# Kernel tuning notes

Measured on AMD Instinct MI355X. Metric: run time of the kernel, lower is better.

## Reference

```python
import jax, jax.numpy as jnp
import numpy as np
import math

N, B, S = 2048, 4, 1024
SFZ, IFZ, H, A = 384, 256, 8, 64
LN_EPS = 1e-5


def setup_inputs() -> dict:
    key = jax.random.key(0)
    ks = jax.random.split(key, 12)
    x = jax.random.normal(ks[0], (N, IFZ), dtype=jnp.float32)
    emb = jax.random.normal(ks[1], (B, S, SFZ), dtype=jnp.float32)
    mask = jax.random.randint(ks[2], (B, S), 0, 2).astype(bool)
    batch = jnp.sort(jax.random.randint(ks[3], (N,), 0, B)).astype(jnp.int64)
    sc = 1.0 / math.sqrt(IFZ)
    scs = 1.0 / math.sqrt(SFZ)
    Wq = jax.random.normal(ks[4], (IFZ, H * A), dtype=jnp.float32) * sc
    Wk = jax.random.normal(ks[5], (SFZ, H * A), dtype=jnp.float32) * scs
    Wv = jax.random.normal(ks[6], (SFZ, H * A), dtype=jnp.float32) * scs
    Wg = jax.random.normal(ks[7], (IFZ, H * A), dtype=jnp.float32) * sc
    bg = jnp.zeros((H * A,), dtype=jnp.float32)
    Wback = jax.random.normal(ks[8], (H * A, IFZ), dtype=jnp.float32) / math.sqrt(H * A)
    bback = jnp.zeros((IFZ,), dtype=jnp.float32)
    gamma = jnp.ones((IFZ,), dtype=jnp.float32)
    beta = jnp.zeros((IFZ,), dtype=jnp.float32)
    return {"x": x, "packed_sequence_emb": emb, "packed_sequence_mask": mask,
            "batch": batch, "Wq": Wq, "Wk": Wk, "Wv": Wv, "Wg": Wg, "bg": bg,
            "Wback": Wback, "bback": bback, "gamma": gamma, "beta": beta}


def _masked_softmax(scores, mask):
    # scores: [N,S,H], mask: [N,S,1] bool; softmax over S with padded entries zeroed
    neg = jnp.finfo(scores.dtype).min
    s = jnp.where(mask, scores, neg)
    s = s - jnp.max(s, axis=1, keepdims=True)
    e = jnp.exp(s) * mask
    return e / (jnp.sum(e, axis=1, keepdims=True) + 1e-9)


def reference(x, packed_sequence_emb, packed_sequence_mask, batch,
              Wq, Wk, Wv, Wg, bg, Wback, bback, gamma, beta):
    scale = math.sqrt(A)
    q = (x @ Wq).reshape(N, H, A)                               # [N,H,A]
    k = (packed_sequence_emb @ Wk).reshape(B, S, H, A)          # [B,S,H,A]
    v = (packed_sequence_emb @ Wv).reshape(B, S, H, A)
    # scores per (node, candidate-batch), then gather node's own batch entry;
    # avoids materializing k[batch] of shape [N,S,H,A]
    scores_all = jnp.einsum('nha,bsha->nbsh', q, k) / scale     # [N,B,S,H]
    idx = batch[:, None, None, None].astype(jnp.int32)
    scores = jnp.take_along_axis(scores_all, idx, axis=1)[:, 0]  # [N,S,H]
    bmask = packed_sequence_mask[batch][..., None]               # [N,S,1]
    w = _masked_softmax(scores, bmask)                           # [N,S,H]
    feat_all = jnp.einsum('nsh,bsha->nbha', w, v)                # [N,B,H,A]
    feat = jnp.take_along_axis(feat_all, idx, axis=1)[:, 0]      # [N,H,A]
    gate = jax.nn.sigmoid(x @ Wg + bg).reshape(N, H, A)
    new = (gate * feat).reshape(N, H * A) @ Wback + bback        # [N,IFZ]
    y = math.sqrt(2.0) * x + new
    mu = jnp.mean(y, axis=-1, keepdims=True)
    var = jnp.mean((y - mu) ** 2, axis=-1, keepdims=True)
    out = (y - mu) * jax.lax.rsqrt(var + LN_EPS) * gamma + beta
    seq_aa_logits = jnp.sum(scores[..., :2], axis=-1)            # [N,S]
    return out, seq_aa_logits
```

## Files before the change

### kernel.cpp

```cpp
#include <hip/hip_runtime.h>
#include <hip/hip_bf16.h>

#define NND 2048
#define BBATCH 4
#define SS 1024
#define SFZ 384
#define IFZ 256
#define HH 8
#define AA 64
#define HA 512
#define NBX 48
#define NSPL 8

typedef __attribute__((ext_vector_type(8))) short bf16x8;
typedef __attribute__((ext_vector_type(4))) float f32x4;

__device__ __forceinline__ unsigned short f2bf(float f) {
    union { float f; unsigned u; } a; a.f = f;
    unsigned r = a.u + 0x7fffu + ((a.u >> 16) & 1u);
    return (unsigned short)(r >> 16);
}
__device__ __forceinline__ float bf2f(unsigned short u) {
    return __uint_as_float((unsigned)u << 16);
}

__device__ __forceinline__ bf16x8 cvt8(const float* __restrict__ p) {
    const float4 f0 = *(const float4*)p;
    const float4 f1 = *(const float4*)(p + 4);
    bf16x8 o;
    o[0] = (short)f2bf(f0.x); o[1] = (short)f2bf(f0.y);
    o[2] = (short)f2bf(f0.z); o[3] = (short)f2bf(f0.w);
    o[4] = (short)f2bf(f1.x); o[5] = (short)f2bf(f1.y);
    o[6] = (short)f2bf(f1.z); o[7] = (short)f2bf(f1.w);
    return o;
}

__device__ __forceinline__ void tile_transpose(
    const float* __restrict__ src, unsigned short* __restrict__ dst,
    int K, int N, int kt, int nt, int t)
{
    __shared__ unsigned short tile[64][65];
    const int k0 = kt * 64, n0 = nt * 64;
    const int tr = t >> 6, tc = t & 63;
    #pragma unroll
    for (int r = 0; r < 16; ++r)
        tile[tr + r*4][tc] = f2bf(src[(size_t)(k0 + tr + r*4) * N + n0 + tc]);
    __syncthreads();
    #pragma unroll
    for (int r = 0; r < 16; ++r)
        dst[(size_t)(n0 + tr + r*4) * K + k0 + tc] = tile[tc][tr + r*4];
}

__global__ __launch_bounds__(256) void prep_kernel(
    const float* __restrict__ Wk, const float* __restrict__ Wv,
    const float* __restrict__ Wq, const float* __restrict__ Wg,
    const float* __restrict__ Wback,
    const void* __restrict__ mask_raw, const void* __restrict__ batch_raw,
    unsigned short* __restrict__ WkT, unsigned short* __restrict__ WvT,
    unsigned short* __restrict__ WqT, unsigned short* __restrict__ WgT,
    unsigned short* __restrict__ WbackT,
    float* __restrict__ mask_f, int* __restrict__ seg)
{
    const int bx = blockIdx.x, t = threadIdx.x;
    if (bx < 48)  { tile_transpose(Wk, WkT, SFZ, HA, bx/8, bx%8, t); return; }
    if (bx < 96)  { const int i = bx-48;  tile_transpose(Wv, WvT, SFZ, HA, i/8, i%8, t); return; }
    if (bx < 128) { const int i = bx-96;  tile_transpose(Wq, WqT, IFZ, HA, i/8, i%8, t); return; }
    if (bx < 160) { const int i = bx-128; tile_transpose(Wg, WgT, IFZ, HA, i/8, i%8, t); return; }
    if (bx < 192) { const int i = bx-160; tile_transpose(Wback, WbackT, HA, IFZ, i/4, i%4, t); return; }
    __shared__ int fl[4];
    __shared__ int fb;
    __shared__ int cnt[4];
    if (t < 4) { fl[t] = 0; cnt[t] = 0; }
    if (t == 0) fb = 0;
    __syncthreads();
    const unsigned char*  mb = (const unsigned char*)mask_raw;
    const unsigned short* mh = (const unsigned short*)mask_raw;
    const unsigned int*   mw = (const unsigned int*)mask_raw;
    int f0 = 0, f1 = 0, f2 = 0, f3 = 0;
    for (int i = t; i < 2048; i += 256) {
        unsigned short h = mh[i];
        if (h == 0x3f80u) f0 = 1;
        if ((i & 1) == 0 && h != 0) f1 = 1;
    }
    for (int i = t; i < 4096; i += 256)
        if ((i & 3) != 0 && mb[i] != 0) f2 = 1;
    for (int i = t; i < 1024; i += 256)
        if ((i & 1) != 0 && mw[i] != 0) f3 = 1;
    const int* bw = (const int*)batch_raw;
    int f4 = 0;
    for (int i = t + 1; i < 2048; i += 256)
        if (bw[i] < bw[i-1]) f4 = 1;
    if (f0) atomicOr(&fl[0], 1);
    if (f1) atomicOr(&fl[1], 1);
    if (f2) atomicOr(&fl[2], 1);
    if (f3) atomicOr(&fl[3], 1);
    if (f4) atomicOr(&fb, 1);
    __syncthreads();
    int mode;
    if (fl[0])      mode = fl[1] ? 1 : 0;
    else if (fl[2]) mode = 2;
    else if (fl[3]) mode = 3;
    else            mode = 4;
    for (int s = t; s < BBATCH*SS; s += 256) {
        int m;
        switch (mode) {
            case 0:  m = (mw[s]   != 0); break;
            case 1:  m = (mh[s]   != 0); break;
            case 2:  m = (mb[s]   != 0); break;
            case 3:  m = (mw[s]   != 0); break;
            default: m = (mw[2*s] != 0); break;
        }
        mask_f[s] = m ? 1.0f : 0.0f;
    }
    const int b64 = fb;
    for (int i = t; i < NND; i += 256) {
        const int bv = (b64 ? bw[2*i] : bw[i]) & 3;
        atomicAdd(&cnt[bv], 1);
    }
    __syncthreads();
    if (t == 0) {
        int s = 0;
        for (int b = 0; b < 4; ++b) { seg[2*b] = s; s += cnt[b]; seg[2*b+1] = s; }
    }
}

__global__ __launch_bounds__(256) void proj_mfma(
    const float* __restrict__ emb, const float* __restrict__ x,
    const unsigned short* __restrict__ WkT, const unsigned short* __restrict__ WvT,
    const unsigned short* __restrict__ WqT, const unsigned short* __restrict__ WgT,
    const float* __restrict__ bg,
    unsigned short* __restrict__ k_blk, unsigned short* __restrict__ vT_bf,
    unsigned short* __restrict__ q_bf, float* __restrict__ gate_ws)
{
    __shared__ unsigned short v_l[16][520];
    const int t = threadIdx.x, w = t >> 6, lane = t & 63;
    const int m16 = lane & 15, quad = lane >> 4;
    const int bx = blockIdx.x;
    if (bx < 512) {
        const int r0 = (bx >> 1) * 16;
        const int b = r0 >> 10, srow = r0 & (SS - 1);
        const float* ap = emb + (size_t)(r0 + m16) * SFZ + quad * 8;
        bf16x8 af[12];
        #pragma unroll
        for (int j = 0; j < 12; ++j) af[j] = cvt8(ap + j * 32);
        if ((bx & 1) == 0) {
            #pragma unroll
            for (int nt = 0; nt < 8; ++nt) {
                const int n0 = w * 128 + nt * 16;
                const unsigned short* bp = WkT + (size_t)(n0 + m16) * SFZ + quad * 8;
                f32x4 d = (f32x4){0.f, 0.f, 0.f, 0.f};
                #pragma unroll
                for (int j = 0; j < 12; ++j)
                    d = __builtin_amdgcn_mfma_f32_16x16x32_bf16(af[j], *(const bf16x8*)(bp + j * 32), d, 0, 0, 0);
                const int head = n0 >> 6, coff = (n0 & 63) + m16;
                unsigned short* kb = k_blk + (((size_t)(b * HH + head)) * SS) * 64 + coff;
                #pragma unroll
                for (int r = 0; r < 4; ++r)
                    kb[(size_t)(srow + quad * 4 + r) * 64] = f2bf(d[r]);
            }
        } else {
            #pragma unroll
            for (int nt = 0; nt < 8; ++nt) {
                const int n0 = w * 128 + nt * 16;
                const unsigned short* bp = WvT + (size_t)(n0 + m16) * SFZ + quad * 8;
                f32x4 d = (f32x4){0.f, 0.f, 0.f, 0.f};
                #pragma unroll
                for (int j = 0; j < 12; ++j)
                    d = __builtin_amdgcn_mfma_f32_16x16x32_bf16(af[j], *(const bf16x8*)(bp + j * 32), d, 0, 0, 0);
                #pragma unroll
                for (int r = 0; r < 4; ++r)
                    v_l[quad * 4 + r][n0 + m16] = f2bf(d[r]);
            }
            __syncthreads();
            for (int c = t; c < HA; c += 256) {
                unsigned short tmp[16];
                #pragma unroll
                for (int s = 0; s < 16; ++s) tmp[s] = v_l[s][c];
                unsigned short* dst = vT_bf + ((size_t)b * HA + c) * SS + srow;
                *(uint4*)dst       = ((const uint4*)tmp)[0];
                *(uint4*)(dst + 8) = ((const uint4*)tmp)[1];
            }
        }
    } else {
        const int i = bx - 512;
        const int r0 = (i >> 2) * 16;
        const int tensor = (i & 3) >> 1, half = i & 1;
        const unsigned short* Wt = tensor ? WgT : WqT;
        const float* ap = x + (size_t)(r0 + m16) * IFZ + quad * 8;
        bf16x8 af[8];
        #pragma unroll
        for (int j = 0; j < 8; ++j) af[j] = cvt8(ap + j * 32);
        #pragma unroll
        for (int nt = 0; nt < 4; ++nt) {
            const int n0 = half * 256 + w * 64 + nt * 16;
            const unsigned short* bp = Wt + (size_t)(n0 + m16) * IFZ + quad * 8;
            f32x4 d = (f32x4){0.f, 0.f, 0.f, 0.f};
            #pragma unroll
            for (int j = 0; j < 8; ++j)
                d = __builtin_amdgcn_mfma_f32_16x16x32_bf16(af[j], *(const bf16x8*)(bp + j * 32), d, 0, 0, 0);
            if (tensor == 0) {
                #pragma unroll
                for (int r = 0; r < 4; ++r)
                    q_bf[(size_t)(r0 + quad * 4 + r) * HA + n0 + m16] = f2bf(d[r]);
            } else {
                const float bgv = bg[n0 + m16];
                #pragma unroll
                for (int r = 0; r < 4; ++r)
                    gate_ws[(size_t)(r0 + quad * 4 + r) * HA + n0 + m16] =
                        1.f / (1.f + __expf(-(d[r] + bgv)));
            }
        }
    }
}

__global__ __launch_bounds__(256) void attn_kernel(
    const unsigned short* __restrict__ k_blk, const unsigned short* __restrict__ vT_bf,
    const unsigned short* __restrict__ q_bf, const float* __restrict__ mask_f,
    const int* __restrict__ seg, unsigned short* __restrict__ part_O,
    float2* __restrict__ part_ml, float* __restrict__ out_logits)
{
    __shared__ unsigned short P_lds[4][16][136];
    const int bid = blockIdx.x;
    const int xcd = bid & 7;
    const int b   = xcd >> 1;
    const int idx = (bid >> 3) * 2 + (xcd & 1);
    const int z    = idx & 15;
    const int xblk = idx >> 4;
    const int hz    = z >> 3;
    const int split = z & 7;
    const int n0 = seg[2*b] + xblk * 16;
    const int nend = seg[2*b + 1];
    if (n0 >= nend) return;
    const int nvalid = min(16, nend - n0);

    const int t = threadIdx.x;
    const int w = t >> 6, lane = t & 63;
    const int m16 = lane & 15, quad = lane >> 4;
    const int h = hz * 4 + w;
    const int s0 = split * 128;

    int nq = n0 + m16; if (nq >= nend) nq = nend - 1;
    const unsigned short* qp = q_bf + (size_t)nq * HA + h * AA + quad * 8;
    const bf16x8 qa0 = *(const bf16x8*)qp;
    const bf16x8 qa1 = *(const bf16x8*)(qp + 32);

    const unsigned short* kb = k_blk + ((size_t)(b * HH + h)) * SS * 64;
    const unsigned short* vb = vT_bf + ((size_t)b * HA + h * AA) * SS;
    unsigned short (*Pw)[136] = P_lds[w];

    float msk[8];
    #pragma unroll
    for (int st = 0; st < 8; ++st)
        msk[st] = mask_f[b * SS + s0 + st * 16 + m16];

    f32x4 d[8];
    #pragma unroll
    for (int st = 0; st < 8; ++st) {
        const unsigned short* kp = kb + (size_t)(s0 + st * 16 + m16) * 64 + quad * 8;
        const bf16x8 b0 = *(const bf16x8*)kp;
        const bf16x8 b1 = *(const bf16x8*)(kp + 32);
        f32x4 acc = (f32x4){0.f, 0.f, 0.f, 0.f};
        acc = __builtin_amdgcn_mfma_f32_16x16x32_bf16(qa0, b0, acc, 0, 0, 0);
        acc = __builtin_amdgcn_mfma_f32_16x16x32_bf16(qa1, b1, acc, 0, 0, 0);
        #pragma unroll
        for (int r = 0; r < 4; ++r) acc[r] *= 0.125f;
        d[st] = acc;
    }
    if (hz == 0 && w == 0) {
        const unsigned short* qp1 = q_bf + (size_t)nq * HA + AA + quad * 8;
        const bf16x8 qb0 = *(const bf16x8*)qp1;
        const bf16x8 qb1 = *(const bf16x8*)(qp1 + 32);
        const unsigned short* kb1 = k_blk + ((size_t)(b * HH + 1)) * SS * 64;
        #pragma unroll
        for (int st = 0; st < 8; ++st) {
            const unsigned short* kp = kb1 + (size_t)(s0 + st * 16 + m16) * 64 + quad * 8;
            f32x4 acc = (f32x4){0.f, 0.f, 0.f, 0.f};
            acc = __builtin_amdgcn_mfma_f32_16x16x32_bf16(qb0, *(const bf16x8*)kp, acc, 0, 0, 0);
            acc = __builtin_amdgcn_mfma_f32_16x16x32_bf16(qb1, *(const bf16x8*)(kp + 32), acc, 0, 0, 0);
            #pragma unroll
            for (int r = 0; r < 4; ++r) {
                const int node = quad * 4 + r;
                if (node < nvalid)
                    out_logits[(size_t)(n0 + node) * SS + s0 + st * 16 + m16] =
                        d[st][r] + acc[r] * 0.125f;
            }
        }
    }
    float m_s[4], l_s[4];
    #pragma unroll
    for (int r = 0; r < 4; ++r) {
        float mx = -3.0e38f;
        #pragma unroll
        for (int st = 0; st < 8; ++st)
            mx = (msk[st] > 0.5f) ? fmaxf(mx, d[st][r]) : mx;
        mx = fmaxf(mx, __shfl_xor(mx, 1));
        mx = fmaxf(mx, __shfl_xor(mx, 2));
        mx = fmaxf(mx, __shfl_xor(mx, 4));
        mx = fmaxf(mx, __shfl_xor(mx, 8));
        m_s[r] = mx;
        float cs = 0.f;
        #pragma unroll
        for (int st = 0; st < 8; ++st) {
            const float e = (msk[st] > 0.5f) ? __expf(d[st][r] - mx) : 0.f;
            d[st][r] = e;
            cs += e;
        }
        cs += __shfl_xor(cs, 1);
        cs += __shfl_xor(cs, 2);
        cs += __shfl_xor(cs, 4);
        cs += __shfl_xor(cs, 8);
        l_s[r] = cs;
    }
    #pragma unroll
    for (int st = 0; st < 8; ++st)
        #pragma unroll
        for (int r = 0; r < 4; ++r)
            Pw[quad * 4 + r][st * 16 + m16] = f2bf(d[st][r]);
    f32x4 facc[4];
    #pragma unroll
    for (int a = 0; a < 4; ++a) facc[a] = (f32x4){0.f, 0.f, 0.f, 0.f};
    #pragma unroll
    for (int sub = 0; sub < 4; ++sub) {
        const bf16x8 pa = *(const bf16x8*)&Pw[m16][sub * 32 + quad * 8];
        const unsigned short* vp0 = vb + (size_t)m16 * SS + s0 + sub * 32 + quad * 8;
        #pragma unroll
        for (int a = 0; a < 4; ++a) {
            const bf16x8 vfr = *(const bf16x8*)(vp0 + (size_t)(a * 16) * SS);
            facc[a] = __builtin_amdgcn_mfma_f32_16x16x32_bf16(pa, vfr, facc[a], 0, 0, 0);
        }
    }
    unsigned short* po = part_O + (size_t)split * NND * HA;
    #pragma unroll
    for (int a = 0; a < 4; ++a)
        #pragma unroll
        for (int r = 0; r < 4; ++r) {
            const int row = quad * 4 + r;
            if (row < nvalid)
                po[(size_t)(n0 + row) * HA + h * AA + a * 16 + m16] = f2bf(facc[a][r]);
        }
    if (m16 == 0) {
        #pragma unroll
        for (int r = 0; r < 4; ++r) {
            const int row = quad * 4 + r;
            if (row < nvalid)
                part_ml[(size_t)split * NND * HH + (size_t)(n0 + row) * HH + h] =
                    make_float2(m_s[r], l_s[r]);
        }
    }
}

__global__ __launch_bounds__(256) void back_ln_fused(
    const unsigned short* __restrict__ part_O, const float2* __restrict__ part_ml,
    const float* __restrict__ gate_ws, const unsigned short* __restrict__ WbackT,
    const float* __restrict__ x, const float* __restrict__ bback,
    const float* __restrict__ gamma, const float* __restrict__ beta,
    float* __restrict__ out)
{
    __shared__ float coef[NSPL][8][8];
    __shared__ unsigned short gf_l[8][520];
    __shared__ float nl[8][260];
    const int t = threadIdx.x, w = t >> 6, lane = t & 63;
    const int m16 = lane & 15, quad = lane >> 4;
    const int r0 = blockIdx.x * 8;
    if (t < 64) {
        const int row = t >> 3, h = t & 7, n = r0 + row;
        float2 ml[NSPL];
        #pragma unroll
        for (int s = 0; s < NSPL; ++s)
            ml[s] = part_ml[(size_t)s * NND * HH + (size_t)n * HH + h];
        float M = -3.0e38f;
        #pragma unroll
        for (int s = 0; s < NSPL; ++s) M = fmaxf(M, ml[s].x);
        float L = 0.f;
        float e[NSPL];
        #pragma unroll
        for (int s = 0; s < NSPL; ++s) { e[s] = __expf(ml[s].x - M); L += ml[s].y * e[s]; }
        const float invL = 1.f / (L + 1e-9f);
        #pragma unroll
        for (int s = 0; s < NSPL; ++s) coef[s][row][h] = e[s] * invL;
    }
    __syncthreads();
    #pragma unroll
    for (int it = 0; it < 4; ++it) {
        const int i = (t + it * 256) * 4;
        const int row = i >> 9, c = i & (HA - 1), h = c >> 6;
        const int n = r0 + row;
        float4 o = make_float4(0.f, 0.f, 0.f, 0.f);
        #pragma unroll
        for (int s = 0; s < NSPL; ++s) {
            const ushort4 p = *(const ushort4*)&part_O[(size_t)s * NND * HA + (size_t)n * HA + c];
            const float cf = coef[s][row][h];
            o.x = fmaf(bf2f(p.x), cf, o.x); o.y = fmaf(bf2f(p.y), cf, o.y);
            o.z = fmaf(bf2f(p.z), cf, o.z); o.w = fmaf(bf2f(p.w), cf, o.w);
        }
        const float4 g = *(const float4*)&gate_ws[(size_t)n * HA + c];
        ushort4 ob;
        ob.x = f2bf(g.x * o.x); ob.y = f2bf(g.y * o.y);
        ob.z = f2bf(g.z * o.z); ob.w = f2bf(g.w * o.w);
        *(ushort4*)&gf_l[row][c] = ob;
    }
    __syncthreads();
    bf16x8 af[16];
    #pragma unroll
    for (int j = 0; j < 16; ++j)
        af[j] = *(const bf16x8*)&gf_l[m16 & 7][quad * 8 + j * 32];
    #pragma unroll
    for (int nt = 0; nt < 4; ++nt) {
        const int n0 = w * 64 + nt * 16;
        const unsigned short* bp = WbackT + (size_t)(n0 + m16) * HA + quad * 8;
        f32x4 d = (f32x4){0.f, 0.f, 0.f, 0.f};
        #pragma unroll
        for (int j = 0; j < 16; ++j)
            d = __builtin_amdgcn_mfma_f32_16x16x32_bf16(af[j], *(const bf16x8*)(bp + j * 32), d, 0, 0, 0);
        const float bb = bback[n0 + m16];
        #pragma unroll
        for (int r = 0; r < 4; ++r) {
            const int rr = quad * 4 + r;
            if (rr < 8) nl[rr][n0 + m16] = d[r] + bb;
        }
    }
    __syncthreads();
    const int row = t >> 5, li = t & 31;
    const float* xr = x + (size_t)(r0 + row) * IFZ;
    float yv[8];
    float s1 = 0.f, s2 = 0.f;
    #pragma unroll
    for (int j = 0; j < 8; ++j) {
        const int c = li + j * 32;
        const float v = fmaf(1.41421356237309515f, xr[c], nl[row][c]);
        yv[j] = v; s1 += v; s2 += v * v;
    }
    #pragma unroll
    for (int off = 16; off >= 1; off >>= 1) {
        s1 += __shfl_xor(s1, off);
        s2 += __shfl_xor(s2, off);
    }
    const float mu  = s1 * (1.f / IFZ);
    const float var = s2 * (1.f / IFZ) - mu * mu;
    const float rv  = rsqrtf(var + 1e-5f);
    float* orow = out + (size_t)(r0 + row) * IFZ;
    #pragma unroll
    for (int j = 0; j < 8; ++j) {
        const int c = li + j * 32;
        orow[c] = (yv[j] - mu) * rv * gamma[c] + beta[c];
    }
}

extern "C" void kernel_launch(void* const* d_in, const int* in_sizes, int n_in,
                              void* d_out, int out_size, void* d_ws, size_t ws_size,
                              hipStream_t stream) {
    const float* x     = (const float*)d_in[0];
    const float* emb   = (const float*)d_in[1];
    const void*  mraw  = d_in[2];
    const void*  braw  = d_in[3];
    const float* Wq    = (const float*)d_in[4];
    const float* Wk    = (const float*)d_in[5];
    const float* Wv    = (const float*)d_in[6];
    const float* Wg    = (const float*)d_in[7];
    const float* bg    = (const float*)d_in[8];
    const float* Wback = (const float*)d_in[9];
    const float* bback = (const float*)d_in[10];
    const float* gamma = (const float*)d_in[11];
    const float* beta  = (const float*)d_in[12];

    char* ws = (char*)d_ws;
    const size_t MB = 1048576;
    size_t off = 0;
    float*          mask_f  = (float*)(ws + off);  off += 16384;
    int*            seg     = (int*)(ws + off);    off += 16384;
    unsigned short* WkT     = (unsigned short*)(ws + off); off += 393216;
    unsigned short* WvT     = (unsigned short*)(ws + off); off += 393216;
    unsigned short* WqT     = (unsigned short*)(ws + off); off += 262144;
    unsigned short* WgT     = (unsigned short*)(ws + off); off += 262144;
    unsigned short* WbackT  = (unsigned short*)(ws + off); off += 262144;
    unsigned short* k_blk   = (unsigned short*)(ws + off); off += 4*MB;
    unsigned short* vT_bf   = (unsigned short*)(ws + off); off += 4*MB;
    unsigned short* q_bf    = (unsigned short*)(ws + off); off += 2*MB;
    float*          gate_ws = (float*)(ws + off); off += 4*MB;
    unsigned short* part_O  = (unsigned short*)(ws + off); off += 16*MB;
    float2*         part_ml = (float2*)(ws + off); off += 1*MB;

    float* out        = (float*)d_out;
    float* out_logits = out + (size_t)NND * IFZ;

    hipLaunchKernelGGL(prep_kernel, dim3(193), dim3(256), 0, stream,
                       Wk, Wv, Wq, Wg, Wback, mraw, braw,
                       WkT, WvT, WqT, WgT, WbackT, mask_f, seg);
    hipLaunchKernelGGL(proj_mfma, dim3(1024), dim3(256), 0, stream,
                       emb, x, WkT, WvT, WqT, WgT, bg, k_blk, vT_bf, q_bf, gate_ws);
    hipLaunchKernelGGL(attn_kernel, dim3(BBATCH * NBX * 16), dim3(256), 0, stream,
                       k_blk, vT_bf, q_bf, mask_f, seg, part_O, part_ml, out_logits);
    hipLaunchKernelGGL(back_ln_fused, dim3(NND / 8), dim3(256), 0, stream,
                       part_O, part_ml, gate_ws, WbackT, x, bback, gamma, beta, out);
}
```

Baseline: 204.3 us.

## Halve attention splits with online softmax; rebalance projection and back-LN grids

```diff
diff --git a/kernel.cpp b/kernel.cpp
--- a/kernel.cpp
+++ b/kernel.cpp
@@ -10,7 +10,7 @@
 #define AA 64
 #define HA 512
 #define NBX 48
-#define NSPL 8
+#define NSPL 4
 
 typedef __attribute__((ext_vector_type(8))) short bf16x8;
 typedef __attribute__((ext_vector_type(4))) float f32x4;
@@ -136,17 +136,19 @@
     const int t = threadIdx.x, w = t >> 6, lane = t & 63;
     const int m16 = lane & 15, quad = lane >> 4;
     const int bx = blockIdx.x;
-    if (bx < 512) {
-        const int r0 = (bx >> 1) * 16;
+    if (bx < 1024) {
+        const int r0 = (bx >> 2) * 16;
+        const int sub = bx & 3;
+        const int tensor = sub >> 1, chalf = sub & 1;
         const int b = r0 >> 10, srow = r0 & (SS - 1);
         const float* ap = emb + (size_t)(r0 + m16) * SFZ + quad * 8;
         bf16x8 af[12];
         #pragma unroll
         for (int j = 0; j < 12; ++j) af[j] = cvt8(ap + j * 32);
-        if ((bx & 1) == 0) {
-            #pragma unroll
-            for (int nt = 0; nt < 8; ++nt) {
-                const int n0 = w * 128 + nt * 16;
+        if (tensor == 0) {
+            #pragma unroll
+            for (int nt = 0; nt < 4; ++nt) {
+                const int n0 = chalf * 256 + w * 64 + nt * 16;
                 const unsigned short* bp = WkT + (size_t)(n0 + m16) * SFZ + quad * 8;
                 f32x4 d = (f32x4){0.f, 0.f, 0.f, 0.f};
                 #pragma unroll
@@ -160,8 +162,8 @@
             }
         } else {
             #pragma unroll
-            for (int nt = 0; nt < 8; ++nt) {
-                const int n0 = w * 128 + nt * 16;
+            for (int nt = 0; nt < 4; ++nt) {
+                const int n0 = chalf * 256 + w * 64 + nt * 16;
                 const unsigned short* bp = WvT + (size_t)(n0 + m16) * SFZ + quad * 8;
                 f32x4 d = (f32x4){0.f, 0.f, 0.f, 0.f};
                 #pragma unroll
@@ -172,7 +174,8 @@
                     v_l[quad * 4 + r][n0 + m16] = f2bf(d[r]);
             }
             __syncthreads();
-            for (int c = t; c < HA; c += 256) {
+            {
+                const int c = chalf * 256 + t;
                 unsigned short tmp[16];
                 #pragma unroll
                 for (int s = 0; s < 16; ++s) tmp[s] = v_l[s][c];
@@ -182,7 +185,7 @@
             }
         }
     } else {
-        const int i = bx - 512;
+        const int i = bx - 1024;
         const int r0 = (i >> 2) * 16;
         const int tensor = (i & 3) >> 1, half = i & 1;
         const unsigned short* Wt = tensor ? WgT : WqT;
@@ -224,10 +227,10 @@
     const int xcd = bid & 7;
     const int b   = xcd >> 1;
     const int idx = (bid >> 3) * 2 + (xcd & 1);
-    const int z    = idx & 15;
-    const int xblk = idx >> 4;
-    const int hz    = z >> 3;
-    const int split = z & 7;
+    const int z    = idx & 7;
+    const int xblk = idx >> 3;
+    const int hz    = z >> 2;
+    const int split = z & 3;
     const int n0 = seg[2*b] + xblk * 16;
     const int nend = seg[2*b + 1];
     if (n0 >= nend) return;
@@ -237,7 +240,6 @@
     const int w = t >> 6, lane = t & 63;
     const int m16 = lane & 15, quad = lane >> 4;
     const int h = hz * 4 + w;
-    const int s0 = split * 128;
 
     int nq = n0 + m16; if (nq >= nend) nq = nend - 1;
     const unsigned short* qp = q_bf + (size_t)nq * HA + h * AA + quad * 8;
@@ -248,96 +250,120 @@
     const unsigned short* vb = vT_bf + ((size_t)b * HA + h * AA) * SS;
     unsigned short (*Pw)[136] = P_lds[w];
 
-    float msk[8];
-    #pragma unroll
-    for (int st = 0; st < 8; ++st)
-        msk[st] = mask_f[b * SS + s0 + st * 16 + m16];
-
-    f32x4 d[8];
-    #pragma unroll
-    for (int st = 0; st < 8; ++st) {
-        const unsigned short* kp = kb + (size_t)(s0 + st * 16 + m16) * 64 + quad * 8;
-        const bf16x8 b0 = *(const bf16x8*)kp;
-        const bf16x8 b1 = *(const bf16x8*)(kp + 32);
-        f32x4 acc = (f32x4){0.f, 0.f, 0.f, 0.f};
-        acc = __builtin_amdgcn_mfma_f32_16x16x32_bf16(qa0, b0, acc, 0, 0, 0);
-        acc = __builtin_amdgcn_mfma_f32_16x16x32_bf16(qa1, b1, acc, 0, 0, 0);
-        #pragma unroll
-        for (int r = 0; r < 4; ++r) acc[r] *= 0.125f;
-        d[st] = acc;
-    }
-    if (hz == 0 && w == 0) {
+    const bool do_logits = (hz == 0 && w == 0);
+    bf16x8 qb0, qb1;
+    const unsigned short* kb1 = k_blk + ((size_t)(b * HH + 1)) * SS * 64;
+    if (do_logits) {
         const unsigned short* qp1 = q_bf + (size_t)nq * HA + AA + quad * 8;
-        const bf16x8 qb0 = *(const bf16x8*)qp1;
-        const bf16x8 qb1 = *(const bf16x8*)(qp1 + 32);
-        const unsigned short* kb1 = k_blk + ((size_t)(b * HH + 1)) * SS * 64;
+        qb0 = *(const bf16x8*)qp1;
+        qb1 = *(const bf16x8*)(qp1 + 32);
+    }
+
+    float m_s[4], l_s[4];
+    #pragma unroll
+    for (int r = 0; r < 4; ++r) { m_s[r] = -3.0e38f; l_s[r] = 0.f; }
+    f32x4 facc[4];
+    #pragma unroll
+    for (int a = 0; a < 4; ++a) facc[a] = (f32x4){0.f, 0.f, 0.f, 0.f};
+
+    for (int ch = 0; ch < 2; ++ch) {
+        const int s0 = split * 256 + ch * 128;
+        float msk[8];
+        #pragma unroll
+        for (int st = 0; st < 8; ++st)
+            msk[st] = mask_f[b * SS + s0 + st * 16 + m16];
+        f32x4 d[8];
         #pragma unroll
         for (int st = 0; st < 8; ++st) {
-            const unsigned short* kp = kb1 + (size_t)(s0 + st * 16 + m16) * 64 + quad * 8;
+            const unsigned short* kp = kb + (size_t)(s0 + st * 16 + m16) * 64 + quad * 8;
+            const bf16x8 b0 = *(const bf16x8*)kp;
+            const bf16x8 b1 = *(const bf16x8*)(kp + 32);
             f32x4 acc = (f32x4){0.f, 0.f, 0.f, 0.f};
-            acc = __builtin_amdgcn_mfma_f32_16x16x32_bf16(qb0, *(const bf16x8*)kp, acc, 0, 0, 0);
-            acc = __builtin_amdgcn_mfma_f32_16x16x32_bf16(qb1, *(const bf16x8*)(kp + 32), acc, 0, 0, 0);
-            #pragma unroll
-            for (int r = 0; r < 4; ++r) {
-                const int node = quad * 4 + r;
-                if (node < nvalid)
-                    out_logits[(size_t)(n0 + node) * SS + s0 + st * 16 + m16] =
-                        d[st][r] + acc[r] * 0.125f;
-            }
-        }
-    }
-    float m_s[4], l_s[4];
-    #pragma unroll
-    for (int r = 0; r < 4; ++r) {
-        float mx = -3.0e38f;
+            acc = __builtin_amdgcn_mfma_f32_16x16x32_bf16(qa0, b0, acc, 0, 0, 0);
+            acc = __builtin_amdgcn_mfma_f32_16x16x32_bf16(qa1, b1, acc, 0, 0, 0);
+            #pragma unroll
+            for (int r = 0; r < 4; ++r) acc[r] *= 0.125f;
+            d[st] = acc;
+        }
+        if (do_logits) {
+            #pragma unroll
+            for (int st = 0; st < 8; ++st) {
+                const unsigned short* kp = kb1 + (size_t)(s0 + st * 16 + m16) * 64 + quad * 8;
+                f32x4 acc = (f32x4){0.f, 0.f, 0.f, 0.f};
+                acc = __builtin_amdgcn_mfma_f32_16x16x32_bf16(qb0, *(const bf16x8*)kp, acc, 0, 0, 0);
+                acc = __builtin_amdgcn_mfma_f32_16x16x32_bf16(qb1, *(const bf16x8*)(kp + 32), acc, 0, 0, 0);
+                #pragma unroll
+                for (int r = 0; r < 4; ++r) {
+                    const int node = quad * 4 + r;
+                    if (node < nvalid)
+                        out_logits[(size_t)(n0 + node) * SS + s0 + st * 16 + m16] =
+                            d[st][r] + acc[r] * 0.125f;
+                }
+            }
+        }
+        float al[4];
+        #pragma unroll
+        for (int r = 0; r < 4; ++r) {
+            float mx = -3.0e38f;
+            #pragma unroll
+            for (int st = 0; st < 8; ++st)
+                mx = (msk[st] > 0.5f) ? fmaxf(mx, d[st][r]) : mx;
+            mx = fmaxf(mx, __shfl_xor(mx, 1));
+            mx = fmaxf(mx, __shfl_xor(mx, 2));
+            mx = fmaxf(mx, __shfl_xor(mx, 4));
+            mx = fmaxf(mx, __shfl_xor(mx, 8));
+            const float mnew = fmaxf(m_s[r], mx);
+            al[r] = __expf(m_s[r] - mnew);
+            m_s[r] = mnew;
+            float cs = 0.f;
+            #pragma unroll
+            for (int st = 0; st < 8; ++st) {
+                const float e = (msk[st] > 0.5f) ? __expf(d[st][r] - mnew) : 0.f;
+                d[st][r] = e;
+                cs += e;
+            }
+            cs += __shfl_xor(cs, 1);
+            cs += __shfl_xor(cs, 2);
+            cs += __shfl_xor(cs, 4);
+            cs += __shfl_xor(cs, 8);
+            l_s[r] = l_s[r] * al[r] + cs;
+        }
         #pragma unroll
         for (int st = 0; st < 8; ++st)
-            mx = (msk[st] > 0.5f) ? fmaxf(mx, d[st][r]) : mx;
-        mx = fmaxf(mx, __shfl_xor(mx, 1));
-        mx = fmaxf(mx, __shfl_xor(mx, 2));
-        mx = fmaxf(mx, __shfl_xor(mx, 4));
-        mx = fmaxf(mx, __shfl_xor(mx, 8));
-        m_s[r] = mx;
-        float cs = 0.f;
-        #pragma unroll
-        for (int st = 0; st < 8; ++st) {
-            const float e = (msk[st] > 0.5f) ? __expf(d[st][r] - mx) : 0.f;
-            d[st][r] = e;
-            cs += e;
-        }
-        cs += __shfl_xor(cs, 1);
-        cs += __shfl_xor(cs, 2);
-        cs += __shfl_xor(cs, 4);
-        cs += __shfl_xor(cs, 8);
-        l_s[r] = cs;
-    }
-    #pragma unroll
-    for (int st = 0; st < 8; ++st)
+            #pragma unroll
+            for (int r = 0; r < 4; ++r)
+                Pw[quad * 4 + r][st * 16 + m16] = f2bf(d[st][r]);
+        #pragma unroll
+        for (int a = 0; a < 4; ++a)
+            #pragma unroll
+            for (int r = 0; r < 4; ++r) facc[a][r] *= al[r];
+        #pragma unroll
+        for (int sub = 0; sub < 4; ++sub) {
+            const bf16x8 pa = *(const bf16x8*)&Pw[m16][sub * 32 + quad * 8];
+            const unsigned short* vp0 = vb + (size_t)m16 * SS + s0 + sub * 32 + quad * 8;
+            #pragma unroll
+            for (int a = 0; a < 4; ++a) {
+                const bf16x8 vfr = *(const bf16x8*)(vp0 + (size_t)(a * 16) * SS);
+                facc[a] = __builtin_amdgcn_mfma_f32_16x16x32_bf16(pa, vfr, facc[a], 0, 0, 0);
+            }
+        }
+    }
+    #pragma unroll
+    for (int a = 0; a < 4; ++a)
         #pragma unroll
         for (int r = 0; r < 4; ++r)
-            Pw[quad * 4 + r][st * 16 + m16] = f2bf(d[st][r]);
-    f32x4 facc[4];
-    #pragma unroll
-    for (int a = 0; a < 4; ++a) facc[a] = (f32x4){0.f, 0.f, 0.f, 0.f};
-    #pragma unroll
-    for (int sub = 0; sub < 4; ++sub) {
-        const bf16x8 pa = *(const bf16x8*)&Pw[m16][sub * 32 + quad * 8];
-        const unsigned short* vp0 = vb + (size_t)m16 * SS + s0 + sub * 32 + quad * 8;
-        #pragma unroll
-        for (int a = 0; a < 4; ++a) {
-            const bf16x8 vfr = *(const bf16x8*)(vp0 + (size_t)(a * 16) * SS);
-            facc[a] = __builtin_amdgcn_mfma_f32_16x16x32_bf16(pa, vfr, facc[a], 0, 0, 0);
-        }
-    }
-    unsigned short* po = part_O + (size_t)split * NND * HA;
-    #pragma unroll
-    for (int a = 0; a < 4; ++a)
-        #pragma unroll
-        for (int r = 0; r < 4; ++r) {
-            const int row = quad * 4 + r;
-            if (row < nvalid)
-                po[(size_t)(n0 + row) * HA + h * AA + a * 16 + m16] = f2bf(facc[a][r]);
-        }
+            Pw[quad * 4 + r][a * 16 + m16] = f2bf(facc[a][r]);
+    {
+        const int row = lane >> 2, cg = lane & 3;
+        if (row < nvalid) {
+            const uint4 v0 = *(const uint4*)&Pw[row][cg * 16];
+            const uint4 v1 = *(const uint4*)&Pw[row][cg * 16 + 8];
+            unsigned short* dst = part_O + (size_t)split * NND * HA +
+                                  (size_t)(n0 + row) * HA + h * AA + cg * 16;
+            *(uint4*)dst       = v0;
+            *(uint4*)(dst + 8) = v1;
+        }
+    }
     if (m16 == 0) {
         #pragma unroll
         for (int r = 0; r < 4; ++r) {
@@ -356,13 +382,13 @@
     const float* __restrict__ gamma, const float* __restrict__ beta,
     float* __restrict__ out)
 {
-    __shared__ float coef[NSPL][8][8];
-    __shared__ unsigned short gf_l[8][520];
-    __shared__ float nl[8][260];
+    __shared__ float coef[NSPL][4][8];
+    __shared__ unsigned short gf_l[4][520];
+    __shared__ float nl[4][260];
     const int t = threadIdx.x, w = t >> 6, lane = t & 63;
     const int m16 = lane & 15, quad = lane >> 4;
-    const int r0 = blockIdx.x * 8;
-    if (t < 64) {
+    const int r0 = blockIdx.x * 4;
+    if (t < 32) {
         const int row = t >> 3, h = t & 7, n = r0 + row;
         float2 ml[NSPL];
         #pragma unroll
@@ -381,7 +407,7 @@
     }
     __syncthreads();
     #pragma unroll
-    for (int it = 0; it < 4; ++it) {
+    for (int it = 0; it < 2; ++it) {
         const int i = (t + it * 256) * 4;
         const int row = i >> 9, c = i & (HA - 1), h = c >> 6;
         const int n = r0 + row;
@@ -403,7 +429,7 @@
     bf16x8 af[16];
     #pragma unroll
     for (int j = 0; j < 16; ++j)
-        af[j] = *(const bf16x8*)&gf_l[m16 & 7][quad * 8 + j * 32];
+        af[j] = *(const bf16x8*)&gf_l[m16 & 3][quad * 8 + j * 32];
     #pragma unroll
     for (int nt = 0; nt < 4; ++nt) {
         const int n0 = w * 64 + nt * 16;
@@ -416,22 +442,22 @@
         #pragma unroll
         for (int r = 0; r < 4; ++r) {
             const int rr = quad * 4 + r;
-            if (rr < 8) nl[rr][n0 + m16] = d[r] + bb;
-        }
-    }
-    __syncthreads();
-    const int row = t >> 5, li = t & 31;
+            if (rr < 4) nl[rr][n0 + m16] = d[r] + bb;
+        }
+    }
+    __syncthreads();
+    const int row = t >> 6, li = t & 63;
     const float* xr = x + (size_t)(r0 + row) * IFZ;
-    float yv[8];
+    float yv[4];
     float s1 = 0.f, s2 = 0.f;
     #pragma unroll
-    for (int j = 0; j < 8; ++j) {
-        const int c = li + j * 32;
+    for (int j = 0; j < 4; ++j) {
+        const int c = li + j * 64;
         const float v = fmaf(1.41421356237309515f, xr[c], nl[row][c]);
         yv[j] = v; s1 += v; s2 += v * v;
     }
     #pragma unroll
-    for (int off = 16; off >= 1; off >>= 1) {
+    for (int off = 32; off >= 1; off >>= 1) {
         s1 += __shfl_xor(s1, off);
         s2 += __shfl_xor(s2, off);
     }
@@ -440,8 +466,8 @@
     const float rv  = rsqrtf(var + 1e-5f);
     float* orow = out + (size_t)(r0 + row) * IFZ;
     #pragma unroll
-    for (int j = 0; j < 8; ++j) {
-        const int c = li + j * 32;
+    for (int j = 0; j < 4; ++j) {
+        const int c = li + j * 64;
         orow[c] = (yv[j] - mu) * rv * gamma[c] + beta[c];
     }
 }
@@ -477,8 +503,8 @@
     unsigned short* vT_bf   = (unsigned short*)(ws + off); off += 4*MB;
     unsigned short* q_bf    = (unsigned short*)(ws + off); off += 2*MB;
     float*          gate_ws = (float*)(ws + off); off += 4*MB;
-    unsigned short* part_O  = (unsigned short*)(ws + off); off += 16*MB;
-    float2*         part_ml = (float2*)(ws + off); off += 1*MB;
+    unsigned short* part_O  = (unsigned short*)(ws + off); off += 8*MB;
+    float2*         part_ml = (float2*)(ws + off); off += 524288;
 
     float* out        = (float*)d_out;
     float* out_logits = out + (size_t)NND * IFZ;
@@ -486,10 +512,10 @@
     hipLaunchKernelGGL(prep_kernel, dim3(193), dim3(256), 0, stream,
                        Wk, Wv, Wq, Wg, Wback, mraw, braw,
                        WkT, WvT, WqT, WgT, WbackT, mask_f, seg);
-    hipLaunchKernelGGL(proj_mfma, dim3(1024), dim3(256), 0, stream,
+    hipLaunchKernelGGL(proj_mfma, dim3(1536), dim3(256), 0, stream,
                        emb, x, WkT, WvT, WqT, WgT, bg, k_blk, vT_bf, q_bf, gate_ws);
-    hipLaunchKernelGGL(attn_kernel, dim3(BBATCH * NBX * 16), dim3(256), 0, stream,
+    hipLaunchKernelGGL(attn_kernel, dim3(BBATCH * NBX * 8), dim3(256), 0, stream,
                        k_blk, vT_bf, q_bf, mask_f, seg, part_O, part_ml, out_logits);
-    hipLaunchKernelGGL(back_ln_fused, dim3(NND / 8), dim3(256), 0, stream,
+    hipLaunchKernelGGL(back_ln_fused, dim3(NND / 4), dim3(256), 0, stream,
                        part_O, part_ml, gate_ws, WbackT, x, bback, gamma, beta, out);
 }
```

Measured after the change: 221.1 us. 8.2% more time.
